# Kernel tuning notes

Measured on AMD Instinct MI355X. Metric: run time of the kernel, lower is better.

The kernel has to match this reference:

```python
import jax, jax.numpy as jnp
import numpy as np

B, N, C, R = 16, 1024, 256, 8
E = 262144
NUM_SUPER = 32
EPS = 1e-5


def _ln(x, g, b):
    mu = jnp.mean(x, axis=-1, keepdims=True)
    var = jnp.var(x, axis=-1, keepdims=True)
    return (x - mu) / jnp.sqrt(var + EPS) * g + b


def setup_inputs() -> dict:
    key = jax.random.key(0)
    ks = jax.random.split(key, 20)

    def w(k, shape, fan_in):
        return (jax.random.normal(k, shape, jnp.float32) / np.sqrt(fan_in)).astype(jnp.float32)

    return dict(
        x=jax.random.normal(ks[0], (B, N, C), jnp.float32),
        batch_edge_index=jax.random.randint(ks[1], (2, E), 0, B * N),
        batch_edge_types=jax.random.randint(ks[2], (E,), 0, R),
        # cross-modal attention
        Wq=w(ks[3], (C, C), C), bq=jnp.zeros((C,), jnp.float32),
        Wk=w(ks[4], (C, C), C), bk=jnp.zeros((C,), jnp.float32),
        Wv=w(ks[5], (C, C), C), bv=jnp.zeros((C,), jnp.float32),
        Wg=w(ks[6], (2 * C, C), 2 * C), bg=jnp.zeros((C,), jnp.float32),
        ln_attn_g=jnp.ones((C,), jnp.float32), ln_attn_b=jnp.zeros((C,), jnp.float32),
        # confidence net
        Wc1=w(ks[7], (C, C // 2), C), bc1=jnp.zeros((C // 2,), jnp.float32),
        Wc2=w(ks[8], (C // 2, 1), C // 2), bc2=jnp.zeros((1,), jnp.float32),
        # feature mixer
        Wm=w(ks[9], (2 * C, C), 2 * C), bm=jnp.zeros((C,), jnp.float32),
        ln1_g=jnp.ones((C,), jnp.float32), ln1_b=jnp.zeros((C,), jnp.float32),
        # RGCN
        W_rel=w(ks[10], (R, C, C), C),
        W_root=w(ks[11], (C, C), C),
        b_rgcn=jnp.zeros((C,), jnp.float32),
        ln2_g=jnp.ones((C,), jnp.float32), ln2_b=jnp.zeros((C,), jnp.float32),
        # super class head
        Wh=w(ks[12], (C, NUM_SUPER), C), bh=jnp.zeros((NUM_SUPER,), jnp.float32),
    )


def reference(x, batch_edge_index, batch_edge_types,
              Wq, bq, Wk, bk, Wv, bv, Wg, bg, ln_attn_g, ln_attn_b,
              Wc1, bc1, Wc2, bc2, Wm, bm, ln1_g, ln1_b,
              W_rel, W_root, b_rgcn, ln2_g, ln2_b, Wh, bh):
    residual = x
    q = x @ Wq + bq
    k = x @ Wk + bk
    v = x @ Wv + bv
    attn = jax.nn.softmax(jnp.einsum('bnc,bmc->bnm', q, k) / jnp.sqrt(jnp.float32(C)), axis=-1)
    out = jnp.einsum('bnm,bmc->bnc', attn, v)
    gate = jax.nn.sigmoid(jnp.concatenate([out, residual], axis=-1) @ Wg + bg)
    validated = _ln(gate * out + (1.0 - gate) * residual, ln_attn_g, ln_attn_b)

    conf = jax.nn.sigmoid(jax.nn.relu(validated @ Wc1 + bc1) @ Wc2 + bc2)  # [B,N,1]
    weighted = validated * conf
    xm = jax.nn.relu(jnp.concatenate([x, weighted], axis=-1) @ Wm + bm)
    xn = _ln(xm, ln1_g, ln1_b).reshape(B * N, C)

    # RGCNConv (PyG defaults: mean aggregation per relation, root weight, bias)
    src, dst = batch_edge_index[0], batch_edge_index[1]
    h = jnp.einsum('nc,rcd->rnd', xn, W_rel)          # [R, B*N, C] relation-transformed nodes
    msg = h[batch_edge_types, src]                    # [E, C] per-edge gather
    seg = dst * R + batch_edge_types                  # (node, relation) segment id
    cnt = jax.ops.segment_sum(jnp.ones((E,), xn.dtype), seg, num_segments=B * N * R)
    msg = msg / jnp.maximum(cnt[seg], 1.0)[:, None]
    agg = jax.ops.segment_sum(msg, dst, num_segments=B * N)
    x_rgcn = agg + xn @ W_root + b_rgcn
    x_rgcn = jax.nn.relu(_ln(x_rgcn.reshape(B, N, C), ln2_g, ln2_b))

    denom = jnp.maximum(conf.sum(axis=1), 1e-8)       # [B,1]
    pooled = (x_rgcn * conf).sum(axis=1) / denom      # [B,C]
    return pooled @ Wh + bh                           # [B, NUM_SUPER]
```

## Files before the change

kernel.cpp:

```cpp
#include <hip/hip_runtime.h>
#include <hip/hip_bf16.h>

#define B_ 16
#define N_ 1024
#define C_ 256
#define R_ 8
#define E_ 262144
#define NS_ 32
#define BN_ (B_*N_)
#define BNC_ (BN_*C_)

typedef __hip_bfloat16 bf16;
typedef __attribute__((ext_vector_type(4))) float f32x4;
typedef __attribute__((ext_vector_type(8))) short bf16x8;

__device__ __forceinline__ float b2f(bf16 x) { return __bfloat162float(x); }
__device__ __forceinline__ bf16  f2b(float x) { return __float2bfloat16(x); }
__device__ __forceinline__ float us2f(unsigned short u) { return __uint_as_float((unsigned)u << 16); }

__device__ __forceinline__ void gload16(const void* g, void* l) {
    auto gp = (const __attribute__((address_space(1))) void*)(unsigned long long)g;
    auto lp = (__attribute__((address_space(3))) void*)(unsigned)(unsigned long long)l;
    __builtin_amdgcn_global_load_lds(gp, lp, 16, 0, 0);
}

template<int ACT>
__global__ __launch_bounds__(256) void gemm_bf16(
    const bf16* __restrict__ A, int lda, long long sA,
    const bf16* __restrict__ Bm, int ldb, long long sB,
    bf16* __restrict__ Cc, int ldc, long long sC,
    const float* __restrict__ bias, const float* __restrict__ bias2,
    const float* __restrict__ bias3, int K)
{
    __shared__ short sbuf[16384];
    const int tid = threadIdx.x;
    const int lane = tid & 63, w = tid >> 6;
    const int wr = w >> 1, wc = w & 1;
    const int bm = blockIdx.y * 128, bn = blockIdx.x * 128;
    const bf16* Ab = A + (size_t)blockIdx.z * sA;
    const bf16* Bb = Bm + (size_t)blockIdx.z * sB;
    bf16* Cb = Cc + (size_t)blockIdx.z * sC;

    const int rg = lane >> 2;
    const int kswz = ((lane & 3) ^ ((rg >> 1) & 3)) * 8;

    f32x4 acc[4][4];
    const f32x4 zz = {0.f, 0.f, 0.f, 0.f};
    #pragma unroll
    for (int i = 0; i < 4; ++i)
        #pragma unroll
        for (int j = 0; j < 4; ++j) acc[i][j] = zz;

    const int fr = lane & 15;
    const int fm = lane >> 4;
    const int fslot = (fm ^ ((fr >> 1) & 3)) * 8;

    const int NI = K >> 5;

#define STAGE_AB(bi, kk) do {                                                          \
    _Pragma("unroll")                                                                  \
    for (int t_ = 0; t_ < 2; ++t_) {                                                   \
        gload16(Ab + (size_t)(bm + t_*64 + w*16 + rg) * lda + (kk) + kswz,             \
                sbuf + (bi)*4096 + t_*2048 + w*512);                                   \
        gload16(Bb + (size_t)(bn + t_*64 + w*16 + rg) * ldb + (kk) + kswz,             \
                sbuf + 8192 + (bi)*4096 + t_*2048 + w*512);                            \
    } } while (0)

    STAGE_AB(0, 0);
    if (NI > 1) STAGE_AB(1, 32);

    for (int i = 0; i < NI; ++i) {
        const int cur = i & 1;
        if (i + 1 < NI) asm volatile("s_waitcnt vmcnt(4)" ::: "memory");
        else            asm volatile("s_waitcnt vmcnt(0)" ::: "memory");
        __builtin_amdgcn_s_barrier();
        __builtin_amdgcn_sched_barrier(0);

        bf16x8 af[4], bfr[4];
        const short* Ac = sbuf + cur * 4096;
        const short* Bc = sbuf + 8192 + cur * 4096;
        #pragma unroll
        for (int ii = 0; ii < 4; ++ii)
            af[ii] = *(const bf16x8*)&Ac[(wr*64 + ii*16 + fr)*32 + fslot];
        #pragma unroll
        for (int jj = 0; jj < 4; ++jj)
            bfr[jj] = *(const bf16x8*)&Bc[(wc*64 + jj*16 + fr)*32 + fslot];

        asm volatile("s_waitcnt lgkmcnt(0)" ::: "memory");
        __builtin_amdgcn_s_barrier();
        __builtin_amdgcn_sched_barrier(0);
        if (i + 2 < NI) STAGE_AB(cur, (i + 2) * 32);

        #pragma unroll
        for (int ii = 0; ii < 4; ++ii)
            #pragma unroll
            for (int jj = 0; jj < 4; ++jj)
                acc[ii][jj] = __builtin_amdgcn_mfma_f32_16x16x32_bf16(af[ii], bfr[jj], acc[ii][jj], 0, 0, 0);
    }
#undef STAGE_AB

    __syncthreads();
    const int er = (lane >> 4) * 4, ec = lane & 15;
    #pragma unroll
    for (int half = 0; half < 2; ++half) {
        if (wr == half) {
            #pragma unroll
            for (int j = 0; j < 4; ++j) {
                const int col = bn + wc*64 + j*16 + ec;
                float bvv = 0.0f;
                if (bias) {
                    const int seg = col >> 8;
                    const float* bp = (seg == 0) ? bias : (seg == 1 ? bias2 : bias3);
                    bvv = bp[col & 255];
                }
                #pragma unroll
                for (int i = 0; i < 4; ++i) {
                    #pragma unroll
                    for (int p = 0; p < 4; ++p) {
                        float val = acc[i][j][p] + bvv;
                        if (ACT == 1) val = fmaxf(val, 0.0f);
                        if (ACT == 2) val = 1.0f / (1.0f + __expf(-val));
                        *(bf16*)&sbuf[(i*16 + er + p)*136 + wc*64 + j*16 + ec] = f2b(val);
                    }
                }
            }
        }
        __syncthreads();
        #pragma unroll
        for (int it = 0; it < 4; ++it) {
            const int ch = tid + it*256;
            const int row = ch >> 4, cp = (ch & 15) * 8;
            *(bf16x8*)&Cb[(size_t)(bm + half*64 + row) * ldc + bn + cp] =
                *(const bf16x8*)&sbuf[row*136 + cp];
        }
        __syncthreads();
    }
}

template<int ACT>
__global__ __launch_bounds__(256) void gemm64_bf16(
    const bf16* __restrict__ A, int lda, long long sA,
    const bf16* __restrict__ Bm, int ldb, long long sB,
    bf16* __restrict__ Cc, int ldc, long long sC,
    const float* __restrict__ bias, int K)
{
    __shared__ short sbuf[8192];
    const int tid = threadIdx.x;
    const int lane = tid & 63, w = tid >> 6;
    const int wr = w >> 1, wc = w & 1;
    const int bm = blockIdx.y * 64, bn = blockIdx.x * 64;
    const bf16* Ab = A + (size_t)blockIdx.z * sA;
    const bf16* Bb = Bm + (size_t)blockIdx.z * sB;
    bf16* Cb = Cc + (size_t)blockIdx.z * sC;

    const int rg = lane >> 2;
    const int kswz = ((lane & 3) ^ ((rg >> 1) & 3)) * 8;

    f32x4 acc[2][2];
    const f32x4 zz = {0.f, 0.f, 0.f, 0.f};
    #pragma unroll
    for (int i = 0; i < 2; ++i)
        #pragma unroll
        for (int j = 0; j < 2; ++j) acc[i][j] = zz;

    const int fr = lane & 15;
    const int fm = lane >> 4;
    const int fslot = (fm ^ ((fr >> 1) & 3)) * 8;

    const int NI = K >> 5;

#define STAGE64(bi, kk) do {                                                           \
    gload16(Ab + (size_t)(bm + w*16 + rg) * lda + (kk) + kswz,                         \
            sbuf + (bi)*2048 + w*512);                                                 \
    gload16(Bb + (size_t)(bn + w*16 + rg) * ldb + (kk) + kswz,                         \
            sbuf + 4096 + (bi)*2048 + w*512);                                          \
    } while (0)

    STAGE64(0, 0);
    if (NI > 1) STAGE64(1, 32);

    for (int i = 0; i < NI; ++i) {
        const int cur = i & 1;
        if (i + 1 < NI) asm volatile("s_waitcnt vmcnt(2)" ::: "memory");
        else            asm volatile("s_waitcnt vmcnt(0)" ::: "memory");
        __builtin_amdgcn_s_barrier();
        __builtin_amdgcn_sched_barrier(0);

        bf16x8 af[2], bfr[2];
        const short* Ac = sbuf + cur * 2048;
        const short* Bc = sbuf + 4096 + cur * 2048;
        #pragma unroll
        for (int ii = 0; ii < 2; ++ii)
            af[ii] = *(const bf16x8*)&Ac[(wr*32 + ii*16 + fr)*32 + fslot];
        #pragma unroll
        for (int jj = 0; jj < 2; ++jj)
            bfr[jj] = *(const bf16x8*)&Bc[(wc*32 + jj*16 + fr)*32 + fslot];

        asm volatile("s_waitcnt lgkmcnt(0)" ::: "memory");
        __builtin_amdgcn_s_barrier();
        __builtin_amdgcn_sched_barrier(0);
        if (i + 2 < NI) STAGE64(cur, (i + 2) * 32);

        #pragma unroll
        for (int ii = 0; ii < 2; ++ii)
            #pragma unroll
            for (int jj = 0; jj < 2; ++jj)
                acc[ii][jj] = __builtin_amdgcn_mfma_f32_16x16x32_bf16(af[ii], bfr[jj], acc[ii][jj], 0, 0, 0);
    }
#undef STAGE64

    __syncthreads();
    const int er = (lane >> 4) * 4, ec = lane & 15;
    #pragma unroll
    for (int j = 0; j < 2; ++j) {
        const int col = bn + wc*32 + j*16 + ec;
        const float bvv = bias ? bias[col & 255] : 0.0f;
        #pragma unroll
        for (int i = 0; i < 2; ++i) {
            #pragma unroll
            for (int p = 0; p < 4; ++p) {
                float val = acc[i][j][p] + bvv;
                if (ACT == 1) val = fmaxf(val, 0.0f);
                if (ACT == 2) val = 1.0f / (1.0f + __expf(-val));
                *(bf16*)&sbuf[(wr*32 + i*16 + er + p)*72 + wc*32 + j*16 + ec] = f2b(val);
            }
        }
    }
    __syncthreads();
    #pragma unroll
    for (int it = 0; it < 2; ++it) {
        const int ch = tid + it*256;
        const int row = ch >> 3, cp = (ch & 7) * 8;
        *(bf16x8*)&Cb[(size_t)(bm + row) * ldc + bn + cp] =
            *(const bf16x8*)&sbuf[row*72 + cp];
    }
}

__global__ __launch_bounds__(256) void prep_w_k(
    const float* __restrict__ Wq, const float* __restrict__ Wk, const float* __restrict__ Wv,
    const float* __restrict__ Wg, const float* __restrict__ Wm, const float* __restrict__ Wc1,
    const float* __restrict__ Wrel, const float* __restrict__ Wroot, bf16* __restrict__ WT)
{
    int t = blockIdx.x;
    const float* in; bf16* out; int K, Nn;
    if (t < 192)      { int wsel = t >> 6; t &= 63;
                        in = wsel == 0 ? Wq : (wsel == 1 ? Wk : Wv);
                        out = WT + wsel*65536; K = 256; Nn = 256; }
    else if (t < 320) { t -= 192; in = Wg;  out = WT + 196608; K = 512; Nn = 256; }
    else if (t < 448) { t -= 320; in = Wm;  out = WT + 327680; K = 512; Nn = 256; }
    else if (t < 480) { t -= 448; in = Wc1; out = WT + 458752; K = 256; Nn = 128; }
    else if (t < 992) { t -= 480; int r = t >> 6; t &= 63;
                        in = Wrel + (size_t)r*65536; out = WT + 491520 + r*65536; K = 256; Nn = 256; }
    else              { t -= 992; in = Wroot; out = WT + 491520 + 524288; K = 256; Nn = 256; }
    const int tpr = Nn >> 5;
    const int n0 = (t % tpr) * 32, k0 = (t / tpr) * 32;
    __shared__ float tile[32][33];
    const int tx = threadIdx.x & 31, ty = threadIdx.x >> 5;
    #pragma unroll
    for (int i = 0; i < 4; ++i) {
        int r = ty + i*8;
        tile[r][tx] = in[(size_t)(k0 + r) * Nn + n0 + tx];
    }
    __syncthreads();
    #pragma unroll
    for (int i = 0; i < 4; ++i) {
        int r = ty + i*8;
        out[(size_t)(n0 + r) * K + k0 + tx] = f2b(tile[tx][r]);
    }
}

__global__ __launch_bounds__(256) void vtrans_k(
    const bf16* __restrict__ in, bf16* __restrict__ out)
{
    __shared__ float tile[32][33];
    in  += (size_t)blockIdx.z * 786432 + 512;
    out += (size_t)blockIdx.z * 262144;
    const int n0 = blockIdx.x * 32, k0 = blockIdx.y * 32;
    const int tx = threadIdx.x & 31, ty = threadIdx.x >> 5;
    #pragma unroll
    for (int i = 0; i < 4; ++i) {
        int r = ty + i*8;
        tile[r][tx] = b2f(in[(size_t)(k0 + r) * 768 + n0 + tx]);
    }
    __syncthreads();
    #pragma unroll
    for (int i = 0; i < 4; ++i) {
        int r = ty + i*8;
        out[(size_t)(n0 + r) * 1024 + k0 + tx] = f2b(tile[tx][r]);
    }
}

__global__ __launch_bounds__(256) void cvt_x_k(const float* __restrict__ x,
    bf16* __restrict__ xb, bf16* __restrict__ cat1, bf16* __restrict__ cat2)
{
    const int i4 = (blockIdx.x * 256 + threadIdx.x) * 4;
    const float4 xv = *(const float4*)(x + i4);
    bf16 bv[4] = { f2b(xv.x), f2b(xv.y), f2b(xv.z), f2b(xv.w) };
    const ushort4 pack = *(const ushort4*)bv;
    const int row = i4 >> 8, col = i4 & 255;
    *(ushort4*)(xb + i4) = pack;
    *(ushort4*)(cat1 + (size_t)row * 512 + 256 + col) = pack;
    *(ushort4*)(cat2 + (size_t)row * 512 + col) = pack;
}

__global__ __launch_bounds__(256) void softmax_k(bf16* __restrict__ s)
{
    const int row = blockIdx.x, tid = threadIdx.x;
    const int lane = tid & 63, wid = tid >> 6;
    bf16* rp = s + (size_t)row * 1024 + tid * 4;
    __shared__ float red[8];
    const ushort4 sv = *(const ushort4*)rp;
    float v0 = us2f(sv.x) * 0.0625f, v1 = us2f(sv.y) * 0.0625f;
    float v2 = us2f(sv.z) * 0.0625f, v3 = us2f(sv.w) * 0.0625f;
    float m = fmaxf(fmaxf(v0, v1), fmaxf(v2, v3));
    #pragma unroll
    for (int o = 32; o >= 1; o >>= 1) m = fmaxf(m, __shfl_xor(m, o));
    if (lane == 0) red[wid] = m;
    __syncthreads();
    const float mx = fmaxf(fmaxf(red[0], red[1]), fmaxf(red[2], red[3]));
    float e0 = __expf(v0 - mx), e1 = __expf(v1 - mx), e2 = __expf(v2 - mx), e3 = __expf(v3 - mx);
    float sm = e0 + e1 + e2 + e3;
    #pragma unroll
    for (int o = 32; o >= 1; o >>= 1) sm += __shfl_xor(sm, o);
    if (lane == 0) red[4 + wid] = sm;
    __syncthreads();
    const float inv = 1.0f / (red[4] + red[5] + red[6] + red[7]);
    bf16 ov[4] = { f2b(e0 * inv), f2b(e1 * inv), f2b(e2 * inv), f2b(e3 * inv) };
    *(ushort4*)rp = *(const ushort4*)ov;
}

template<int RELU>
__global__ __launch_bounds__(256) void ln_k(
    const bf16* __restrict__ in, bf16* __restrict__ out,
    const float* __restrict__ g, const float* __restrict__ bta)
{
    const int node = blockIdx.x * 4 + (threadIdx.x >> 6);
    const int lane = threadIdx.x & 63;
    const ushort4 iv = *(const ushort4*)(in + (size_t)node * 256 + lane * 4);
    float v0 = us2f(iv.x), v1 = us2f(iv.y), v2 = us2f(iv.z), v3 = us2f(iv.w);
    float s  = v0 + v1 + v2 + v3;
    float sq = v0*v0 + v1*v1 + v2*v2 + v3*v3;
    #pragma unroll
    for (int o = 32; o >= 1; o >>= 1) { s += __shfl_xor(s, o); sq += __shfl_xor(sq, o); }
    const float mean = s * (1.0f / 256.0f);
    const float var  = sq * (1.0f / 256.0f) - mean * mean;
    const float rs = rsqrtf(var + 1e-5f);
    const float4 gv = *(const float4*)(g + lane * 4);
    const float4 bv = *(const float4*)(bta + lane * 4);
    float y0 = (v0 - mean) * rs * gv.x + bv.x;
    float y1 = (v1 - mean) * rs * gv.y + bv.y;
    float y2 = (v2 - mean) * rs * gv.z + bv.z;
    float y3 = (v3 - mean) * rs * gv.w + bv.w;
    if (RELU) { y0 = fmaxf(y0, 0.f); y1 = fmaxf(y1, 0.f); y2 = fmaxf(y2, 0.f); y3 = fmaxf(y3, 0.f); }
    bf16 ov[4] = { f2b(y0), f2b(y1), f2b(y2), f2b(y3) };
    *(ushort4*)(out + (size_t)node * 256 + lane * 4) = *(const ushort4*)ov;
}

__global__ __launch_bounds__(256) void blend_ln_k(
    const bf16* __restrict__ gate, const bf16* __restrict__ cat1,
    const float* __restrict__ x, bf16* __restrict__ valid,
    const float* __restrict__ g, const float* __restrict__ bta)
{
    const int node = blockIdx.x * 4 + (threadIdx.x >> 6);
    const int lane = threadIdx.x & 63;
    const ushort4 gt4 = *(const ushort4*)(gate + (size_t)node * 256 + lane * 4);
    const ushort4 ao4 = *(const ushort4*)(cat1 + (size_t)node * 512 + lane * 4);
    const float4  xv4 = *(const float4*)(x + (size_t)node * 256 + lane * 4);
    float g0 = us2f(gt4.x), g1 = us2f(gt4.y), g2 = us2f(gt4.z), g3 = us2f(gt4.w);
    float v0 = g0 * us2f(ao4.x) + (1.f - g0) * xv4.x;
    float v1 = g1 * us2f(ao4.y) + (1.f - g1) * xv4.y;
    float v2 = g2 * us2f(ao4.z) + (1.f - g2) * xv4.z;
    float v3 = g3 * us2f(ao4.w) + (1.f - g3) * xv4.w;
    float s  = v0 + v1 + v2 + v3;
    float sq = v0*v0 + v1*v1 + v2*v2 + v3*v3;
    #pragma unroll
    for (int o = 32; o >= 1; o >>= 1) { s += __shfl_xor(s, o); sq += __shfl_xor(sq, o); }
    const float mean = s * (1.0f / 256.0f);
    const float var  = sq * (1.0f / 256.0f) - mean * mean;
    const float rs = rsqrtf(var + 1e-5f);
    const float4 gv = *(const float4*)(g + lane * 4);
    const float4 bv = *(const float4*)(bta + lane * 4);
    bf16 ov[4] = { f2b((v0 - mean) * rs * gv.x + bv.x), f2b((v1 - mean) * rs * gv.y + bv.y),
                   f2b((v2 - mean) * rs * gv.z + bv.z), f2b((v3 - mean) * rs * gv.w + bv.w) };
    *(ushort4*)(valid + (size_t)node * 256 + lane * 4) = *(const ushort4*)ov;
}

__global__ __launch_bounds__(256) void conf_w_k(
    const bf16* __restrict__ t1, const float* __restrict__ Wc2, const float* __restrict__ bc2,
    const bf16* __restrict__ valid, float* __restrict__ conf, bf16* __restrict__ cat2)
{
    const int node = blockIdx.x * 4 + (threadIdx.x >> 6);
    const int lane = threadIdx.x & 63;
    float a = b2f(t1[(size_t)node * 128 + lane]) * Wc2[lane]
            + b2f(t1[(size_t)node * 128 + 64 + lane]) * Wc2[64 + lane];
    #pragma unroll
    for (int o = 32; o >= 1; o >>= 1) a += __shfl_xor(a, o);
    const float c = 1.0f / (1.0f + __expf(-(a + bc2[0])));
    if (lane == 0) conf[node] = c;
    const ushort4 vv = *(const ushort4*)(valid + (size_t)node * 256 + lane * 4);
    bf16 ov[4] = { f2b(us2f(vv.x) * c), f2b(us2f(vv.y) * c), f2b(us2f(vv.z) * c), f2b(us2f(vv.w) * c) };
    *(ushort4*)(cat2 + (size_t)node * 512 + 256 + lane * 4) = *(const ushort4*)ov;
}

__global__ __launch_bounds__(256) void count2_k(
    const int* __restrict__ dst, const int* __restrict__ et,
    int* __restrict__ deg, int* __restrict__ cnt8)
{
    const int e = blockIdx.x * 256 + threadIdx.x;
    if (e < E_) {
        const int d = dst[e];
        atomicAdd(&deg[d], 1);
        atomicAdd(&cnt8[d * 8 + et[e]], 1);
    }
}

__global__ __launch_bounds__(256) void scan_k(
    const int* __restrict__ deg, int* __restrict__ rowptr, int* __restrict__ cursor)
{
    __shared__ int part[256];
    const int tid = threadIdx.x;
    const int base = tid * 64;
    int s = 0;
    for (int i = 0; i < 64; ++i) s += deg[base + i];
    part[tid] = s; __syncthreads();
    for (int off = 1; off < 256; off <<= 1) {
        int t = (tid >= off) ? part[tid - off] : 0;
        __syncthreads();
        part[tid] += t;
        __syncthreads();
    }
    int run = (tid == 0) ? 0 : part[tid - 1];
    for (int i = 0; i < 64; ++i) {
        rowptr[base + i] = run;
        cursor[base + i] = run;
        run += deg[base + i];
    }
    if (tid == 255) rowptr[BN_] = run;
}

__global__ __launch_bounds__(256) void fill_k(
    const int* __restrict__ src, const int* __restrict__ dst, const int* __restrict__ et,
    int* __restrict__ cursor, int* __restrict__ elist)
{
    const int e = blockIdx.x * 256 + threadIdx.x;
    if (e < E_) {
        const int pos = atomicAdd(&cursor[dst[e]], 1);
        elist[pos] = src[e] | (et[e] << 16);
    }
}

__global__ __launch_bounds__(256) void gather_ln_k(
    const int* __restrict__ rowptr, const int* __restrict__ elist,
    const bf16* __restrict__ h, const int* __restrict__ cnt8,
    const float* __restrict__ brg,
    const float* __restrict__ g, const float* __restrict__ bta,
    bf16* __restrict__ xr)
{
    const int node = blockIdx.x * 4 + (threadIdx.x >> 6);
    const int lane = threadIdx.x & 63;
    const int e0 = rowptr[node], e1 = rowptr[node + 1];
    float invc[8];
    #pragma unroll
    for (int r = 0; r < 8; ++r)
        invc[r] = 1.0f / fmaxf((float)cnt8[node * 8 + r], 1.0f);
    float a0 = 0.f, a1 = 0.f, a2 = 0.f, a3 = 0.f;
    for (int e = e0; e < e1; ++e) {
        const int pe = elist[e];
        const int srcn = pe & 0xffff, rel = pe >> 16;
        const float wgt = invc[rel];
        const ushort4 hv = *(const ushort4*)(h + (size_t)srcn * 2304 + rel * 256 + lane * 4);
        a0 += wgt * us2f(hv.x); a1 += wgt * us2f(hv.y);
        a2 += wgt * us2f(hv.z); a3 += wgt * us2f(hv.w);
    }
    const ushort4 rv = *(const ushort4*)(h + (size_t)node * 2304 + 2048 + lane * 4);
    const float4 bg4 = *(const float4*)(brg + lane * 4);
    const float v0 = a0 + us2f(rv.x) + bg4.x, v1 = a1 + us2f(rv.y) + bg4.y;
    const float v2 = a2 + us2f(rv.z) + bg4.z, v3 = a3 + us2f(rv.w) + bg4.w;
    float s  = v0 + v1 + v2 + v3;
    float sq = v0*v0 + v1*v1 + v2*v2 + v3*v3;
    #pragma unroll
    for (int m = 32; m >= 1; m >>= 1) { s += __shfl_xor(s, m); sq += __shfl_xor(sq, m); }
    const float mean = s * (1.0f / 256.0f);
    const float var  = sq * (1.0f / 256.0f) - mean * mean;
    const float rs = rsqrtf(var + 1e-5f);
    const float4 gv = *(const float4*)(g + lane * 4);
    const float4 bv = *(const float4*)(bta + lane * 4);
    bf16 tb[4] = { f2b(fmaxf((v0 - mean) * rs * gv.x + bv.x, 0.f)),
                   f2b(fmaxf((v1 - mean) * rs * gv.y + bv.y, 0.f)),
                   f2b(fmaxf((v2 - mean) * rs * gv.z + bv.z, 0.f)),
                   f2b(fmaxf((v3 - mean) * rs * gv.w + bv.w, 0.f)) };
    *(ushort4*)(xr + (size_t)node * 256 + lane * 4) = *(const ushort4*)tb;
}

__global__ __launch_bounds__(256) void pool1_k(
    const bf16* __restrict__ xr, const float* __restrict__ conf, float* __restrict__ partial)
{
    const int b = blockIdx.x, chunk = blockIdx.y, c = threadIdx.x;
    float acc = 0.0f;
    for (int n = 0; n < 64; ++n) {
        const int node = b * 1024 + chunk * 64 + n;
        acc += conf[node] * b2f(xr[(size_t)node * 256 + c]);
    }
    partial[(size_t)(b * 16 + chunk) * 256 + c] = acc;
}

__global__ __launch_bounds__(256) void pool2_k(
    const float* __restrict__ partial, const float* __restrict__ conf,
    const float* __restrict__ Wh, const float* __restrict__ bh, float* __restrict__ out)
{
    const int b = blockIdx.x, tid = threadIdx.x;
    __shared__ float red[256];
    __shared__ float pooled[256];
    float pc = 0.0f;
    for (int ch = 0; ch < 16; ++ch) pc += partial[(size_t)(b * 16 + ch) * 256 + tid];
    float s = conf[b * 1024 + tid] + conf[b * 1024 + 256 + tid]
            + conf[b * 1024 + 512 + tid] + conf[b * 1024 + 768 + tid];
    red[tid] = s; __syncthreads();
    for (int st = 128; st > 0; st >>= 1) { if (tid < st) red[tid] += red[tid + st]; __syncthreads(); }
    const float denom = fmaxf(red[0], 1e-8f);
    pooled[tid] = pc / denom;
    __syncthreads();
    if (tid < NS_) {
        float o = bh[tid];
        for (int c = 0; c < 256; ++c) o += pooled[c] * Wh[c * NS_ + tid];
        out[b * NS_ + tid] = o;
    }
}

extern "C" void kernel_launch(void* const* d_in, const int* in_sizes, int n_in,
                              void* d_out, int out_size, void* d_ws, size_t ws_size,
                              hipStream_t stream) {
    const float* x    = (const float*)d_in[0];
    const int*   ei   = (const int*)d_in[1];
    const int*   et   = (const int*)d_in[2];
    const float* Wq   = (const float*)d_in[3];  const float* bq  = (const float*)d_in[4];
    const float* Wk   = (const float*)d_in[5];  const float* bk  = (const float*)d_in[6];
    const float* Wv   = (const float*)d_in[7];  const float* bv  = (const float*)d_in[8];
    const float* Wg   = (const float*)d_in[9];  const float* bg  = (const float*)d_in[10];
    const float* lag  = (const float*)d_in[11]; const float* lab = (const float*)d_in[12];
    const float* Wc1  = (const float*)d_in[13]; const float* bc1 = (const float*)d_in[14];
    const float* Wc2  = (const float*)d_in[15]; const float* bc2 = (const float*)d_in[16];
    const float* Wm   = (const float*)d_in[17]; const float* bm  = (const float*)d_in[18];
    const float* l1g  = (const float*)d_in[19]; const float* l1b = (const float*)d_in[20];
    const float* Wrel = (const float*)d_in[21]; const float* Wroot = (const float*)d_in[22];
    const float* brg  = (const float*)d_in[23];
    const float* l2g  = (const float*)d_in[24]; const float* l2b = (const float*)d_in[25];
    const float* Wh   = (const float*)d_in[26]; const float* bh  = (const float*)d_in[27];
    const int* esrc = ei;
    const int* edst = ei + E_;

    char* w8 = (char*)d_ws;
    bf16*  qkv   = (bf16*)(w8 + 0);
    bf16*  hbuf  = (bf16*)(w8 + 0);
    bf16*  sP    = (bf16*)(w8 + 25165824);
    bf16*  cat1  = (bf16*)(w8 + 58720256);
    bf16*  cat2  = (bf16*)(w8 + 75497472);
    bf16*  gate  = (bf16*)(w8 + 92274688);
    bf16*  valid = (bf16*)(w8 + 100663296);
    bf16*  t1    = (bf16*)(w8 + 109051904);
    bf16*  xm    = (bf16*)(w8 + 113246208);
    bf16*  xb    = (bf16*)(w8 + 121634816);
    bf16*  xn    = (bf16*)(w8 + 130023424);
    bf16*  vtb   = (bf16*)(w8 + 138412032);
    bf16*  xr    = (bf16*)(w8 + 146800640);
    float* conf  = (float*)(w8 + 155189248);
    float* part  = (float*)(w8 + 155254784);
    bf16*  WT    = (bf16*)(w8 + 155516928);
    int*  deg    = (int*)(w8 + 157679616);
    int*  cnt8i  = (int*)(w8 + 157745152);
    int*  rowptr = (int*)(w8 + 158269440);
    int*  cursor = (int*)(w8 + 158335232);
    int*  elist  = (int*)(w8 + 158400768);
    bf16* WqkvT = WT;
    bf16* WgT   = WT + 196608;
    bf16* WmT   = WT + 327680;
    bf16* Wc1T  = WT + 458752;
    bf16* WBIG  = WT + 491520;
    float* outp = (float*)d_out;

    dim3 blk(256);

    prep_w_k<<<1056, blk, 0, stream>>>(Wq, Wk, Wv, Wg, Wm, Wc1, Wrel, Wroot, WT);
    cvt_x_k<<<BNC_ / 1024, blk, 0, stream>>>(x, xb, cat1, cat2);
    hipMemsetAsync(deg, 0, 589824, stream);
    count2_k<<<E_ / 256, blk, 0, stream>>>(edst, et, deg, cnt8i);
    scan_k<<<1, blk, 0, stream>>>(deg, rowptr, cursor);
    fill_k<<<E_ / 256, blk, 0, stream>>>(esrc, edst, et, cursor, elist);

    gemm_bf16<0><<<dim3(6, 128, 1), blk, 0, stream>>>(
        xb, 256, 0, WqkvT, 256, 0, qkv, 768, 0, bq, bk, bv, 256);
    vtrans_k<<<dim3(8, 32, 16), blk, 0, stream>>>(qkv, vtb);

    gemm_bf16<0><<<dim3(8, 8, 16), blk, 0, stream>>>(
        qkv, 768, 786432, qkv + 256, 768, 786432, sP, 1024, 1048576, nullptr, nullptr, nullptr, 256);
    softmax_k<<<BN_, blk, 0, stream>>>(sP);
    gemm64_bf16<0><<<dim3(4, 16, 16), blk, 0, stream>>>(
        sP, 1024, 1048576, vtb, 1024, 262144, cat1, 512, 524288, nullptr, 1024);

    gemm64_bf16<2><<<dim3(4, 256, 1), blk, 0, stream>>>(
        cat1, 512, 0, WgT, 512, 0, gate, 256, 0, bg, 512);
    blend_ln_k<<<BN_ / 4, blk, 0, stream>>>(gate, cat1, x, valid, lag, lab);

    gemm64_bf16<1><<<dim3(2, 256, 1), blk, 0, stream>>>(
        valid, 256, 0, Wc1T, 256, 0, t1, 128, 0, bc1, 256);
    conf_w_k<<<BN_ / 4, blk, 0, stream>>>(t1, Wc2, bc2, valid, conf, cat2);

    gemm64_bf16<1><<<dim3(4, 256, 1), blk, 0, stream>>>(
        cat2, 512, 0, WmT, 512, 0, xm, 256, 0, bm, 512);
    ln_k<0><<<BN_ / 4, blk, 0, stream>>>(xm, xn, l1g, l1b);

    gemm_bf16<0><<<dim3(18, 128, 1), blk, 0, stream>>>(
        xn, 256, 0, WBIG, 256, 0, hbuf, 2304, 0, nullptr, nullptr, nullptr, 256);
    gather_ln_k<<<BN_ / 4, blk, 0, stream>>>(rowptr, elist, hbuf, cnt8i, brg, l2g, l2b, xr);

    pool1_k<<<dim3(B_, 16), blk, 0, stream>>>(xr, conf, part);
    pool2_k<<<B_, blk, 0, stream>>>(part, conf, Wh, bh, outp);
}
```

Baseline: 289.2 us.

## Remap GEMM tiles for XCD locality, deepen pipeline, unroll gather, retile PV

New measurement: 263.8 us. 1.1x faster.

```diff
diff --git a/kernel.cpp b/kernel.cpp
--- a/kernel.cpp
+++ b/kernel.cpp
@@ -36,7 +36,13 @@
     const int tid = threadIdx.x;
     const int lane = tid & 63, w = tid >> 6;
     const int wr = w >> 1, wc = w & 1;
-    const int bm = blockIdx.y * 128, bn = blockIdx.x * 128;
+
+    const int gx = gridDim.x;
+    const int nwg = gx * gridDim.y;
+    int id = blockIdx.y * gx + blockIdx.x;
+    if ((nwg & 7) == 0) { const int cpx = nwg >> 3; id = (id & 7) * cpx + (id >> 3); }
+    const int bm = (id / gx) * 128, bn = (id % gx) * 128;
+
     const bf16* Ab = A + (size_t)blockIdx.z * sA;
     const bf16* Bb = Bm + (size_t)blockIdx.z * sB;
     bf16* Cb = Cc + (size_t)blockIdx.z * sC;
@@ -144,11 +150,17 @@
     bf16* __restrict__ Cc, int ldc, long long sC,
     const float* __restrict__ bias, int K)
 {
-    __shared__ short sbuf[8192];
+    __shared__ short sbuf[16384];
     const int tid = threadIdx.x;
     const int lane = tid & 63, w = tid >> 6;
     const int wr = w >> 1, wc = w & 1;
-    const int bm = blockIdx.y * 64, bn = blockIdx.x * 64;
+
+    const int gx = gridDim.x;
+    const int nwg = gx * gridDim.y;
+    int id = blockIdx.y * gx + blockIdx.x;
+    if ((nwg & 7) == 0) { const int cpx = nwg >> 3; id = (id & 7) * cpx + (id >> 3); }
+    const int bm = (id / gx) * 64, bn = (id % gx) * 64;
+
     const bf16* Ab = A + (size_t)blockIdx.z * sA;
     const bf16* Bb = Bm + (size_t)blockIdx.z * sB;
     bf16* Cb = Cc + (size_t)blockIdx.z * sC;
@@ -173,22 +185,26 @@
     gload16(Ab + (size_t)(bm + w*16 + rg) * lda + (kk) + kswz,                         \
             sbuf + (bi)*2048 + w*512);                                                 \
     gload16(Bb + (size_t)(bn + w*16 + rg) * ldb + (kk) + kswz,                         \
-            sbuf + 4096 + (bi)*2048 + w*512);                                          \
+            sbuf + 8192 + (bi)*2048 + w*512);                                          \
     } while (0)
 
     STAGE64(0, 0);
     if (NI > 1) STAGE64(1, 32);
+    if (NI > 2) STAGE64(2, 64);
+    if (NI > 3) STAGE64(3, 96);
 
     for (int i = 0; i < NI; ++i) {
-        const int cur = i & 1;
-        if (i + 1 < NI) asm volatile("s_waitcnt vmcnt(2)" ::: "memory");
-        else            asm volatile("s_waitcnt vmcnt(0)" ::: "memory");
+        const int cur = i & 3;
+        if (i + 3 < NI)      asm volatile("s_waitcnt vmcnt(6)" ::: "memory");
+        else if (i + 2 < NI) asm volatile("s_waitcnt vmcnt(4)" ::: "memory");
+        else if (i + 1 < NI) asm volatile("s_waitcnt vmcnt(2)" ::: "memory");
+        else                 asm volatile("s_waitcnt vmcnt(0)" ::: "memory");
         __builtin_amdgcn_s_barrier();
         __builtin_amdgcn_sched_barrier(0);
 
         bf16x8 af[2], bfr[2];
         const short* Ac = sbuf + cur * 2048;
-        const short* Bc = sbuf + 4096 + cur * 2048;
+        const short* Bc = sbuf + 8192 + cur * 2048;
         #pragma unroll
         for (int ii = 0; ii < 2; ++ii)
             af[ii] = *(const bf16x8*)&Ac[(wr*32 + ii*16 + fr)*32 + fslot];
@@ -199,7 +215,7 @@
         asm volatile("s_waitcnt lgkmcnt(0)" ::: "memory");
         __builtin_amdgcn_s_barrier();
         __builtin_amdgcn_sched_barrier(0);
-        if (i + 2 < NI) STAGE64(cur, (i + 2) * 32);
+        if (i + 4 < NI) STAGE64(cur, (i + 4) * 32);
 
         #pragma unroll
         for (int ii = 0; ii < 2; ++ii)
@@ -464,11 +480,21 @@
     for (int r = 0; r < 8; ++r)
         invc[r] = 1.0f / fmaxf((float)cnt8[node * 8 + r], 1.0f);
     float a0 = 0.f, a1 = 0.f, a2 = 0.f, a3 = 0.f;
-    for (int e = e0; e < e1; ++e) {
+    int e = e0;
+    for (; e + 1 < e1; e += 2) {
+        const int pe0 = elist[e], pe1 = elist[e + 1];
+        const float w0 = invc[pe0 >> 16], w1 = invc[pe1 >> 16];
+        const ushort4 hv0 = *(const ushort4*)(h + (size_t)(pe0 & 0xffff) * 2304 + (pe0 >> 16) * 256 + lane * 4);
+        const ushort4 hv1 = *(const ushort4*)(h + (size_t)(pe1 & 0xffff) * 2304 + (pe1 >> 16) * 256 + lane * 4);
+        a0 += w0 * us2f(hv0.x) + w1 * us2f(hv1.x);
+        a1 += w0 * us2f(hv0.y) + w1 * us2f(hv1.y);
+        a2 += w0 * us2f(hv0.z) + w1 * us2f(hv1.z);
+        a3 += w0 * us2f(hv0.w) + w1 * us2f(hv1.w);
+    }
+    if (e < e1) {
         const int pe = elist[e];
-        const int srcn = pe & 0xffff, rel = pe >> 16;
-        const float wgt = invc[rel];
-        const ushort4 hv = *(const ushort4*)(h + (size_t)srcn * 2304 + rel * 256 + lane * 4);
+        const float wgt = invc[pe >> 16];
+        const ushort4 hv = *(const ushort4*)(h + (size_t)(pe & 0xffff) * 2304 + (pe >> 16) * 256 + lane * 4);
         a0 += wgt * us2f(hv.x); a1 += wgt * us2f(hv.y);
         a2 += wgt * us2f(hv.z); a3 += wgt * us2f(hv.w);
     }
@@ -594,8 +620,8 @@
     gemm_bf16<0><<<dim3(8, 8, 16), blk, 0, stream>>>(
         qkv, 768, 786432, qkv + 256, 768, 786432, sP, 1024, 1048576, nullptr, nullptr, nullptr, 256);
     softmax_k<<<BN_, blk, 0, stream>>>(sP);
-    gemm64_bf16<0><<<dim3(4, 16, 16), blk, 0, stream>>>(
-        sP, 1024, 1048576, vtb, 1024, 262144, cat1, 512, 524288, nullptr, 1024);
+    gemm_bf16<0><<<dim3(2, 8, 16), blk, 0, stream>>>(
+        sP, 1024, 1048576, vtb, 1024, 262144, cat1, 512, 524288, nullptr, nullptr, nullptr, 1024);
 
     gemm64_bf16<2><<<dim3(4, 256, 1), blk, 0, stream>>>(
         cat1, 512, 0, WgT, 512, 0, gate, 256, 0, bg, 512);
```
